# Kernel tuning notes

Measured on AMD Instinct MI355X. Metric: run time of the kernel, lower is better.

Reference implementation:

```python
import jax, jax.numpy as jnp
from jax import lax
import numpy as np

ANCHOR_SCALES = [8, 16, 32]
ANCHOR_RATIOS = [0.5, 1.0, 2.0]
NUM_ANCHOR = len(ANCHOR_SCALES) * len(ANCHOR_RATIOS)
NMS_THRESH = 0.5


def _base_anchors(base_size=16):
    # generate_anchor_in_cell (called with defaults in the torch code)
    a = []
    for s in ANCHOR_SCALES:
        for r in ANCHOR_RATIOS:
            w = base_size * s * np.sqrt(r)
            h = w / r
            xmin = base_size / 2 - w / 2
            ymin = base_size / 2 - h / 2
            a.append([xmin, ymin, xmin + w, ymin + h])
    return np.array(a, dtype=np.float32)  # (A,4)


def _anchors_in_image(H, W, feature_stride):
    base = _base_anchors(16)  # torch code uses default stride for the base cell
    gx = np.arange(0, feature_stride * W, feature_stride)
    gy = np.arange(0, feature_stride * H, feature_stride)
    gx, gy = np.meshgrid(gx, gy)
    grid = np.stack([gx.ravel(), gy.ravel(), gx.ravel(), gy.ravel()], axis=1)  # (K,4)
    anc = (grid[:, None, :] + base[None, :, :]).reshape(-1, 4)  # (K*A,4)
    return jnp.asarray(anc, dtype=jnp.float32)


def _loc2bbox(anchors, loc):
    # anchors: (N,4) xyxy; loc: (B,N,4) (dx,dy,dw,dh)
    w = anchors[:, 2] - anchors[:, 0]
    h = anchors[:, 3] - anchors[:, 1]
    cx = anchors[:, 0] + 0.5 * w
    cy = anchors[:, 1] + 0.5 * h
    dx, dy, dw, dh = loc[..., 0], loc[..., 1], loc[..., 2], loc[..., 3]
    ncx = dx * w + cx
    ncy = dy * h + cy
    nw = jnp.exp(dw) * w
    nh = jnp.exp(dh) * h
    return jnp.stack([ncx - 0.5 * nw, ncy - 0.5 * nh,
                      ncx + 0.5 * nw, ncy + 0.5 * nh], axis=-1)


def _clip_bbox(rois, img_h, img_w):
    x = jnp.clip(rois[..., 0::2], 0.0, img_w)
    y = jnp.clip(rois[..., 1::2], 0.0, img_h)
    out = jnp.stack([x[..., 0], y[..., 0], x[..., 1], y[..., 1]], axis=-1)
    return out


def _nms(boxes, scores, thresh):
    # Greedy NMS. Returns (boxes_sorted_by_score, keep_mask) of fixed shape.
    N = boxes.shape[0]
    order = jnp.argsort(-scores)
    b = boxes[order]
    x1, y1, x2, y2 = b[:, 0], b[:, 1], b[:, 2], b[:, 3]
    areas = (x2 - x1) * (y2 - y1)
    idx = jnp.arange(N)

    def body(i, state):
        suppressed, keep = state
        cur = jnp.logical_not(suppressed[i])
        keep = keep.at[i].set(cur)
        bi = b[i]
        xx1 = jnp.maximum(bi[0], x1)
        yy1 = jnp.maximum(bi[1], y1)
        xx2 = jnp.minimum(bi[2], x2)
        yy2 = jnp.minimum(bi[3], y2)
        inter = jnp.maximum(xx2 - xx1, 0.0) * jnp.maximum(yy2 - yy1, 0.0)
        iou = inter / (areas[i] + areas - inter)
        sup = (iou > thresh) & cur & (idx > i)
        return (suppressed | sup, keep)

    suppressed0 = jnp.zeros((N,), dtype=bool)
    keep0 = jnp.zeros((N,), dtype=bool)
    _, keep = lax.fori_loop(0, N, body, (suppressed0, keep0))
    return b, keep, order


def reference(feature_map, feature_stride, conv_w, conv_b, score_w, score_b, loc_w, loc_b):
    B, C, H, W = feature_map.shape
    anchors = _anchors_in_image(H, W, feature_stride)  # (H*W*A, 4)

    dn = ('NCHW', 'OIHW', 'NCHW')
    mid = jax.nn.relu(lax.conv_general_dilated(
        feature_map, conv_w, (1, 1), ((1, 1), (1, 1)), dimension_numbers=dn)
        + conv_b[None, :, None, None])
    rpn_score = lax.conv_general_dilated(mid, score_w, (1, 1), ((0, 0), (0, 0)),
                                         dimension_numbers=dn) + score_b[None, :, None, None]
    rpn_loc = lax.conv_general_dilated(mid, loc_w, (1, 1), ((0, 0), (0, 0)),
                                       dimension_numbers=dn) + loc_b[None, :, None, None]

    # NCHW -> NHWC -> (B,H,W,A,2), softmax over the 2 classes
    rpn_score = jnp.transpose(rpn_score, (0, 2, 3, 1)).reshape(B, H, W, NUM_ANCHOR, 2)
    rpn_score = jax.nn.softmax(rpn_score, axis=4)
    rpn_loc = jnp.transpose(rpn_loc, (0, 2, 3, 1)).reshape(B, -1, 4)
    rpn_fg_score = rpn_score[..., 1].reshape(B, -1)
    rpn_score = rpn_score.reshape(B, -1, 2)

    rois = _loc2bbox(anchors, rpn_loc)                      # (B,N,4)
    rois = _clip_bbox(rois, H * feature_stride, W * feature_stride)

    # torch code flattens scores across batch -> effectively B == 1
    flat_rois = rois.reshape(-1, 4)
    flat_scores = rpn_fg_score.reshape(-1)
    b_sorted, keep, _ = _nms(lax.stop_gradient(flat_rois),
                             lax.stop_gradient(flat_scores), NMS_THRESH)
    # compacted kept rois (kept first, zero padding) at fixed shape
    order = jnp.argsort(-flat_scores)
    comp = jnp.argsort(~keep)  # stable: kept positions first
    rois_out = (flat_rois[order][comp] * keep[comp][:, None].astype(flat_rois.dtype))

    return rois_out, keep[comp], anchors, rpn_loc, rpn_score


def setup_inputs() -> dict:
    key = jax.random.key(0)
    k1, k2, k3, k4 = jax.random.split(key, 4)
    C_in, C_mid, A = 2048, 256, NUM_ANCHOR
    H, W = 38, 50
    feature_map = jax.random.normal(k1, (1, C_in, H, W), dtype=jnp.float32)
    conv_w = jax.random.normal(k2, (C_mid, C_in, 3, 3), dtype=jnp.float32) * 0.01
    conv_b = jnp.zeros((C_mid,), dtype=jnp.float32)
    score_w = jax.random.normal(k3, (A * 2, C_mid, 1, 1), dtype=jnp.float32) * 0.01
    score_b = jnp.zeros((A * 2,), dtype=jnp.float32)
    loc_w = jax.random.normal(k4, (A * 4, C_mid, 1, 1), dtype=jnp.float32) * 0.01
    loc_b = jnp.zeros((A * 4,), dtype=jnp.float32)
    return {"feature_map": feature_map, "feature_stride": 16,
            "conv_w": conv_w, "conv_b": conv_b,
            "score_w": score_w, "score_b": score_b,
            "loc_w": loc_w, "loc_b": loc_b}
```

## Files before the change

kernel.cpp:

```cpp
#include <hip/hip_runtime.h>
#include <cstdint>

#define U64 unsigned long long

static constexpr int H = 38, W = 50, P = 1900;
static constexpr int CIN = 2048, CMID = 256;
static constexpr int NA = 9, NBOX = 17100;
static constexpr int HP = 40, WP = 52, QP = HP * WP;
static constexpr int TPITCH = 2084;
static constexpr int KS = 7;
static constexpr int NW = 268;
static constexpr int PITCH = 17152;
static constexpr float NMS_T = 0.5f;
static constexpr int QTILE = 256;

static constexpr size_t SZ_INT  = (size_t)CIN * TPITCH * 4;
static constexpr size_t SZ_WT   = (size_t)9 * CIN * CMID * 4;
static constexpr size_t SZ_PART = (size_t)KS * P * CMID * 4;
static constexpr size_t OFF_INT  = 0;
static constexpr size_t OFF_WT   = OFF_INT + SZ_INT;
static constexpr size_t OFF_PART = OFF_WT + SZ_WT;
static constexpr size_t REGA     = OFF_PART + SZ_PART;
static constexpr size_t OFF_MASK = 0;
static constexpr size_t OFF_MID  = REGA;
static constexpr size_t OFF_FG   = OFF_MID + 1945600;
static constexpr size_t OFF_BOX  = OFF_FG + 68608;
static constexpr size_t OFF_SBOX = OFF_BOX + 273664;
static constexpr size_t OFF_SAREA= OFF_SBOX + 273664;
static constexpr size_t OFF_CNT  = OFF_SAREA + 68608;
static constexpr size_t WS_NEED  = OFF_CNT + 68608;

__device__ __forceinline__ U64 rdlane64(U64 v, int l) {
    unsigned lo = (unsigned)__builtin_amdgcn_readlane((int)(unsigned)(v & 0xffffffffull), l);
    unsigned hi = (unsigned)__builtin_amdgcn_readlane((int)(unsigned)(v >> 32), l);
    return ((U64)hi << 32) | (U64)lo;
}


__global__ __launch_bounds__(256) void k_sentinel(float* out, int n) {
    int i = blockIdx.x * 256 + threadIdx.x;
    if (i < n) out[i] = 1.2345678e8f;
}

__global__ __launch_bounds__(256) void k_in_t(const float* __restrict__ fm, float* __restrict__ in_tT) {
    int idx = blockIdx.x * 256 + threadIdx.x;
    if (idx >= CIN * (H * W)) return;
    int ci = idx / (H * W), hw = idx - ci * (H * W);
    int h = hw / W, w = hw - h * W;
    in_tT[(size_t)ci * TPITCH + (h + 1) * WP + 1 + w] = fm[idx];
}

__global__ __launch_bounds__(256) void k_w_t(const float* __restrict__ cw, float* __restrict__ w2) {
    int idx = blockIdx.x * 256 + threadIdx.x;
    if (idx >= CMID * CIN * 9) return;
    int co = idx / (CIN * 9);
    int rem = idx - co * (CIN * 9);
    int ci = rem / 9, k = rem - ci * 9;
    w2[((size_t)(co >> 3) * CIN + ci) * 72 + k * 8 + (co & 7)] = cw[idx];
}

__global__ __launch_bounds__(256, 2) void k_conv(const float* __restrict__ in_tT,
                                                 const float* __restrict__ w2,
                                                 float* __restrict__ partial) {
    __shared__ float4 s_in4[16 * 104];
    int t = threadIdx.x;
    int lane = t & 63;
    int sub = __builtin_amdgcn_readfirstlane(t >> 6);

    int raw = blockIdx.x;
    int xcd = raw & 7, i0 = raw >> 3;
    int L = xcd * 63 + i0;
    int z = L / 72;
    int r0 = L - z * 72;
    int bx = r0 % 9, by = r0 / 9;
    int q0 = bx * QTILE;
    int cout0 = by * 32;
    int cin0 = (z <= 1) ? 304 * z : 608 + 288 * (z - 2);
    int cin1 = cin0 + ((z <= 1) ? 304 : 288);

    float acc[4][8];
#pragma unroll
    for (int j = 0; j < 4; ++j)
#pragma unroll
        for (int c = 0; c < 8; ++c) acc[j][c] = 0.f;

    const float* wbase = w2 + (size_t)(by * 4 + sub) * CIN * 72;

    for (int c0 = cin0; c0 < cin1; c0 += 16) {
        for (int idx = t; idx < 16 * 92; idx += 256) {
            int r = idx / 92, j = idx - r * 92;
            int qf = q0 - 56 + 4 * j;
            float4 v = make_float4(0.f, 0.f, 0.f, 0.f);
            if (qf >= 0 && qf <= 2080)
                v = *reinterpret_cast<const float4*>(in_tT + (size_t)(c0 + r) * TPITCH + qf);
            s_in4[r * 104 + j + (j >> 3)] = v;
        }
        __syncthreads();
#pragma unroll 1
        for (int r = 0; r < 16; ++r) {
            const float4* row4 = s_in4 + r * 104;
            const float4* w4 = reinterpret_cast<const float4*>(wbase + (size_t)(c0 + r) * 72);
#pragma unroll
            for (int dy = 0; dy < 3; ++dy) {
                int v0 = lane + 13 * dy;
                int v1 = v0 + 1, v2 = v0 + 2;
                float4 F0 = row4[v0 + (v0 >> 3)];
                float4 F1 = row4[v1 + (v1 >> 3)];
                float4 F2 = row4[v2 + (v2 >> 3)];
                float F[12] = {F0.x, F0.y, F0.z, F0.w, F1.x, F1.y, F1.z, F1.w,
                               F2.x, F2.y, F2.z, F2.w};
#pragma unroll
                for (int dxi = 0; dxi < 3; ++dxi) {
                    int k = dy * 3 + dxi;
                    float4 wa = w4[k * 2], wb = w4[k * 2 + 1];
                    float wv[8] = {wa.x, wa.y, wa.z, wa.w, wb.x, wb.y, wb.z, wb.w};
#pragma unroll
                    for (int jj = 0; jj < 4; ++jj) {
                        float iv = F[jj + dxi + 3];
#pragma unroll
                        for (int c = 0; c < 8; ++c) acc[jj][c] += iv * wv[c];
                    }
                }
            }
        }
        __syncthreads();
    }
    float* part = partial + (size_t)z * P * CMID;
#pragma unroll
    for (int jj = 0; jj < 4; ++jj) {
        int q = q0 + 4 * lane + jj;
        if (q < QP) {
            int hp = q / WP, wp_ = q - hp * WP;
            if (hp >= 1 && hp <= H && wp_ >= 1 && wp_ <= W) {
                int p = (hp - 1) * W + (wp_ - 1);
                float* dst = part + (size_t)p * CMID + cout0 + sub * 8;
                float4* d4 = reinterpret_cast<float4*>(dst);
                d4[0] = make_float4(acc[jj][0], acc[jj][1], acc[jj][2], acc[jj][3]);
                d4[1] = make_float4(acc[jj][4], acc[jj][5], acc[jj][6], acc[jj][7]);
            }
        }
    }
}

__global__ __launch_bounds__(256) void k_reduce(const float* __restrict__ partial,
                                                const float* __restrict__ bias,
                                                float* __restrict__ mid) {
    int p = blockIdx.x, c = threadIdx.x;
    float s = bias[c];
    for (int ks = 0; ks < KS; ++ks) s += partial[(size_t)ks * P * CMID + (size_t)p * CMID + c];
    mid[(size_t)p * CMID + c] = fmaxf(s, 0.f);
}

__global__ __launch_bounds__(256) void k_heads(const float* __restrict__ mid,
                                               const float* __restrict__ score_w,
                                               const float* __restrict__ score_b,
                                               const float* __restrict__ loc_w,
                                               const float* __restrict__ loc_b,
                                               float* __restrict__ score_out,
                                               float* __restrict__ loc_out,
                                               float* __restrict__ anch_out,
                                               float* __restrict__ fg,
                                               float* __restrict__ boxes) {
    __shared__ float wl[256][56];
    __shared__ float bias[56];
    __shared__ float dots[4][64];
    int t = threadIdx.x;
    for (int idx = t; idx < 18 * 256; idx += 256) {
        int c = idx >> 8, i = idx & 255;
        wl[i][c] = score_w[idx];
    }
    for (int idx = t; idx < 36 * 256; idx += 256) {
        int c = idx >> 8, i = idx & 255;
        wl[i][18 + c] = loc_w[idx];
    }
    if (t < 18) bias[t] = score_b[t];
    else if (t < 54) bias[t] = loc_b[t - 18];
    __syncthreads();

    int pl = t >> 6, c = t & 63;
    for (int rep = 0; rep < 4; ++rep) {
        int p = blockIdx.x * 16 + rep * 4 + pl;
        if (c < 54 && p < P) {
            float d = bias[c];
            const float4* mp = reinterpret_cast<const float4*>(mid + (size_t)p * CMID);
            for (int i4 = 0; i4 < 64; ++i4) {
                float4 m4 = mp[i4];
                int i = i4 * 4;
                d += m4.x * wl[i][c] + m4.y * wl[i + 1][c] + m4.z * wl[i + 2][c] + m4.w * wl[i + 3][c];
            }
            dots[pl][c] = d;
        }
        __syncthreads();
        if (c < NA && p < P) {
            int a = c;
            int idx = p * NA + a;
            float l0 = dots[pl][2 * a], l1 = dots[pl][2 * a + 1];
            float mx = fmaxf(l0, l1);
            float e0 = expf(l0 - mx), e1 = expf(l1 - mx);
            float den = e0 + e1;
            float s0 = e0 / den, s1 = e1 / den;
            score_out[(size_t)idx * 2 + 0] = s0;
            score_out[(size_t)idx * 2 + 1] = s1;
            fg[idx] = s1;
            float dx = dots[pl][18 + 4 * a + 0];
            float dy = dots[pl][18 + 4 * a + 1];
            float dw = dots[pl][18 + 4 * a + 2];
            float dh = dots[pl][18 + 4 * a + 3];
            loc_out[(size_t)idx * 4 + 0] = dx;
            loc_out[(size_t)idx * 4 + 1] = dy;
            loc_out[(size_t)idx * 4 + 2] = dw;
            loc_out[(size_t)idx * 4 + 3] = dh;
            int hh = p / W, ww = p % W;
            const double scales[3] = {8.0, 16.0, 32.0};
            const double ratios[3] = {0.5, 1.0, 2.0};
            double s = scales[a / 3], r = ratios[a % 3];
            double wb2 = 16.0 * s * sqrt(r);
            double hb = wb2 / r;
            double xmin = 8.0 - wb2 / 2.0, ymin = 8.0 - hb / 2.0;
            float b0 = (float)xmin, b1 = (float)ymin;
            float b2 = (float)(xmin + wb2), b3 = (float)(ymin + hb);
            float gx = (float)(ww * 16), gy = (float)(hh * 16);
            float a0 = gx + b0, a1 = gy + b1, a2 = gx + b2, a3 = gy + b3;
            anch_out[(size_t)idx * 4 + 0] = a0;
            anch_out[(size_t)idx * 4 + 1] = a1;
            anch_out[(size_t)idx * 4 + 2] = a2;
            anch_out[(size_t)idx * 4 + 3] = a3;
            float aw = a2 - a0, ah = a3 - a1;
            float cx = a0 + 0.5f * aw, cy = a1 + 0.5f * ah;
            float ncx = dx * aw + cx, ncy = dy * ah + cy;
            float nw = expf(dw) * aw, nh = expf(dh) * ah;
            float x1 = ncx - 0.5f * nw, y1 = ncy - 0.5f * nh;
            float x2 = ncx + 0.5f * nw, y2 = ncy + 0.5f * nh;
            x1 = fminf(fmaxf(x1, 0.f), (float)(W * 16));
            x2 = fminf(fmaxf(x2, 0.f), (float)(W * 16));
            y1 = fminf(fmaxf(y1, 0.f), (float)(H * 16));
            y2 = fminf(fmaxf(y2, 0.f), (float)(H * 16));
            float4* bp = reinterpret_cast<float4*>(boxes);
            bp[idx] = make_float4(x1, y1, x2, y2);
        }
        __syncthreads();
    }
}

static constexpr int JSL = 2144;
__global__ __launch_bounds__(256) void k_rank_part(const float* __restrict__ fg,
                                                   int* __restrict__ cntb) {
    __shared__ float4 tile[256];
    int t = threadIdx.x;
    int i = blockIdx.x * 256 + t;
    int j0 = blockIdx.y * JSL;
    int j1 = min(NBOX, j0 + JSL);
    float my = (i < NBOX) ? fg[i] : 0.f;
    int cnt = 0;
    for (int base = j0; base < j1; base += 1024) {
        int j = base + t * 4;
        float4 v = make_float4(-3.4e38f, -3.4e38f, -3.4e38f, -3.4e38f);
        if (j + 3 < j1) {
            v = *reinterpret_cast<const float4*>(fg + j);
        } else {
            if (j < j1) v.x = fg[j];
            if (j + 1 < j1) v.y = fg[j + 1];
            if (j + 2 < j1) v.z = fg[j + 2];
            if (j + 3 < j1) v.w = fg[j + 3];
        }
        __syncthreads();
        tile[t] = v;
        __syncthreads();
        if (i < NBOX) {
            for (int u = 0; u < 256; ++u) {
                float4 s = tile[u];
                int jb = base + u * 4;
                cnt += (s.x > my) || (s.x == my && jb < i);
                cnt += (s.y > my) || (s.y == my && jb + 1 < i);
                cnt += (s.z > my) || (s.z == my && jb + 2 < i);
                cnt += (s.w > my) || (s.w == my && jb + 3 < i);
            }
        }
    }
    if (i < NBOX && cnt) atomicAdd(&cntb[i], cnt);
}

__global__ __launch_bounds__(256) void k_scatter(const int* __restrict__ cntb,
                                                 const float* __restrict__ boxes,
                                                 float* __restrict__ sboxes,
                                                 float* __restrict__ sarea) {
    int i = blockIdx.x * 256 + threadIdx.x;
    if (i >= NBOX) return;
    int c = cntb[i];
    float4 b = reinterpret_cast<const float4*>(boxes)[i];
    reinterpret_cast<float4*>(sboxes)[c] = b;
    sarea[c] = (b.z - b.x) * (b.w - b.y);
}

__global__ __launch_bounds__(256) void k_maskfill(const float* __restrict__ sboxes,
                                                  const float* __restrict__ sarea,
                                                  U64* __restrict__ maskT) {
    int w = blockIdx.y;
    int i0 = blockIdx.x * 256;
    if (w < (i0 >> 6)) return;
    __shared__ float4 sb[64];
    __shared__ float sa[64];
    int t = threadIdx.x;
    if (t < 64) {
        int j = w * 64 + t;
        if (j < NBOX) {
            sb[t] = reinterpret_cast<const float4*>(sboxes)[j];
            sa[t] = sarea[j];
        } else {
            sb[t] = make_float4(0.f, 0.f, 0.f, 0.f);
            sa[t] = 0.f;
        }
    }
    __syncthreads();
    int i = i0 + t;
    if (i >= NBOX || w < (i >> 6)) return;
    float4 bi = reinterpret_cast<const float4*>(sboxes)[i];
    float ai = sarea[i];
    U64 word = 0;
#pragma unroll 4
    for (int jb = 0; jb < 64; ++jb) {
        int j = w * 64 + jb;
        float4 bj = sb[jb];
        float xx1 = fmaxf(bi.x, bj.x), yy1 = fmaxf(bi.y, bj.y);
        float xx2 = fminf(bi.z, bj.z), yy2 = fminf(bi.w, bj.w);
        float inter = fmaxf(xx2 - xx1, 0.f) * fmaxf(yy2 - yy1, 0.f);
        float iou = inter / (ai + sa[jb] - inter);
        word |= ((U64)((iou > NMS_T) && (j > i))) << jb;
    }
    maskT[(size_t)w * PITCH + i] = word;
}

__global__ __launch_bounds__(256) void k_sweep(const U64* __restrict__ maskT,
                                               const float* __restrict__ sboxes,
                                               float* __restrict__ rois_out,
                                               float* __restrict__ keep_out) {
    __shared__ U64 rem[NW];
    __shared__ int klbuf[2][64];
    __shared__ int kn[2];
    __shared__ unsigned base_s;
    int t = threadIdx.x;
    for (int u = t; u < NW; u += 256) rem[u] = 0;
    if (t == 0) { base_s = 0; kn[0] = 0; kn[1] = 0; }

    U64 dA = 0, nA = 0, dB = 0, nB = 0;
    if (t < 64) {
        int r0 = t;
        dA = maskT[(size_t)0 * PITCH + r0];
        nA = maskT[(size_t)1 * PITCH + r0];
        int r1 = 64 + t;
        dB = maskT[(size_t)1 * PITCH + r1];
        nB = maskT[(size_t)2 * PITCH + r1];
    }
    __syncthreads();

    auto body = [&](int g, U64& dR, U64& nR) {
        if (t < 64) {
            int nv = min(64, NBOX - g * 64);
            U64 vmask = (nv == 64) ? ~0ull : ((1ull << nv) - 1);
            U64 m = rem[g];
            U64 notsup = ~m & vmask;
            U64 kept = 0;
            while (notsup) {
                int i = (int)__builtin_ctzll(notsup);
                kept |= (1ull << i);
                U64 wi = rdlane64(dR, i);
                notsup &= ~(wi | (1ull << i));
            }
            int nk = __popcll(kept);
            bool mine = (kept >> t) & 1ull;

            U64 val = mine ? nR : 0;
#pragma unroll
            for (int s = 1; s < 64; s <<= 1) val |= (U64)__shfl_xor((unsigned long long)val, s, 64);
            if (t == 0 && g + 1 < NW && val) atomicOr(&rem[g + 1], val);

            if (g + 2 < NW) {
                int row = (g + 2) * 64 + t;
                dR = (row < NBOX) ? maskT[(size_t)(g + 2) * PITCH + row] : 0;
                nR = (row < NBOX && g + 3 < NW) ? maskT[(size_t)(g + 3) * PITCH + row] : 0;
            }

            unsigned base = base_s;
            if (mine) {
                unsigned pre = (unsigned)__popcll(kept & ((1ull << t) - 1));
                unsigned dst = base + pre;
                float4 bb = reinterpret_cast<const float4*>(sboxes)[g * 64 + t];
                reinterpret_cast<float4*>(rois_out)[dst] = bb;
                keep_out[dst] = 1.0f;
                klbuf[g & 1][pre] = t;
            }
            if (t == 0) {
                kn[g & 1] = nk;
                base_s = base + (unsigned)nk;
            }
        } else if (g >= 1) {
            int pb = (g - 1) & 1;
            int nkp = kn[pb];
            if (nkp) {
                const size_t colbase = (size_t)(g - 1) * 64;
                for (int w = g + 1 + (t - 64); w < NW; w += 192) {
                    const U64* col = maskT + (size_t)w * PITCH + colbase;
                    U64 acc = 0;
                    int b = 0;
                    for (; b + 3 < nkp; b += 4) {
                        U64 v0 = col[klbuf[pb][b]];
                        U64 v1 = col[klbuf[pb][b + 1]];
                        U64 v2 = col[klbuf[pb][b + 2]];
                        U64 v3 = col[klbuf[pb][b + 3]];
                        acc |= v0 | v1 | v2 | v3;
                    }
                    for (; b < nkp; ++b) acc |= col[klbuf[pb][b]];
                    if (acc) atomicOr(&rem[w], acc);
                }
            }
        }
        __syncthreads();
    };

    for (int gg = 0; gg < NW; gg += 2) {
        body(gg, dA, nA);
        body(gg + 1, dB, nB);
    }
}

extern "C" void kernel_launch(void* const* d_in, const int* in_sizes, int n_in,
                              void* d_out, int out_size, void* d_ws, size_t ws_size,
                              hipStream_t stream) {
    const float* fm      = (const float*)d_in[0];
    const float* conv_w  = (const float*)d_in[2];
    const float* conv_b  = (const float*)d_in[3];
    const float* score_w = (const float*)d_in[4];
    const float* score_b = (const float*)d_in[5];
    const float* loc_w   = (const float*)d_in[6];
    const float* loc_b   = (const float*)d_in[7];

    float* out = (float*)d_out;
    float* rois_out  = out;
    float* keep_out  = out + NBOX * 4;
    float* anch_out  = out + NBOX * 5;
    float* loc_out   = out + NBOX * 9;
    float* score_out = out + NBOX * 13;

    if (ws_size < WS_NEED) {
        k_sentinel<<<(out_size + 255) / 256, 256, 0, stream>>>(out, out_size);
        return;
    }

    char* ws = (char*)d_ws;
    float* in_tT   = (float*)(ws + OFF_INT);
    float* w2      = (float*)(ws + OFF_WT);
    float* partial = (float*)(ws + OFF_PART);
    U64*   maskT   = (U64*)(ws + OFF_MASK);
    float* mid     = (float*)(ws + OFF_MID);
    float* fg      = (float*)(ws + OFF_FG);
    float* boxes   = (float*)(ws + OFF_BOX);
    float* sboxes  = (float*)(ws + OFF_SBOX);
    float* sarea   = (float*)(ws + OFF_SAREA);
    int*   cntb    = (int*)(ws + OFF_CNT);

    hipMemsetAsync(in_tT, 0, SZ_INT, stream);
    k_in_t<<<(CIN * H * W + 255) / 256, 256, 0, stream>>>(fm, in_tT);
    k_w_t<<<(CMID * CIN * 9 + 255) / 256, 256, 0, stream>>>(conv_w, w2);
    k_conv<<<504, 256, 0, stream>>>(in_tT, w2, partial);
    k_reduce<<<P, 256, 0, stream>>>(partial, conv_b, mid);
    k_heads<<<(P + 15) / 16, 256, 0, stream>>>(mid, score_w, score_b, loc_w, loc_b,
                                               score_out, loc_out, anch_out, fg, boxes);
    hipMemsetAsync(cntb, 0, NBOX * 4, stream);
    k_rank_part<<<dim3((NBOX + 255) / 256, 8), 256, 0, stream>>>(fg, cntb);
    k_scatter<<<(NBOX + 255) / 256, 256, 0, stream>>>(cntb, boxes, sboxes, sarea);
    hipMemsetAsync(rois_out, 0, (size_t)NBOX * 5 * 4, stream);
    k_maskfill<<<dim3((NBOX + 255) / 256, NW), 256, 0, stream>>>(sboxes, sarea, maskT);
    k_sweep<<<1, 256, 0, stream>>>(maskT, sboxes, rois_out, keep_out);
}
```

Before: 852.5 us.

## Store NMS mask row-major and sweep kept rows with coalesced lane-parallel reads

Changes the IoU suppression mask from a column-major (word-major) layout to a row-major layout with a stride of 272 words per box. The single-block sweep now assigns each kept box of the previous group to a wavefront, whose lanes read consecutive words of that box's row and OR them into the shared remove mask. The old version did gathered strided column reads per word. This aims to make the serial sweep's global reads contiguous. In exchange, maskfill writes become strided by 272 words per thread, and there are many more shared-memory atomics, one per nonzero word.

```diff
diff --git a/kernel.cpp b/kernel.cpp
--- a/kernel.cpp
+++ b/kernel.cpp
@@ -10,7 +10,7 @@
 static constexpr int TPITCH = 2084;
 static constexpr int KS = 7;
 static constexpr int NW = 268;
-static constexpr int PITCH = 17152;
+static constexpr int MSTRIDE = 272;
 static constexpr float NMS_T = 0.5f;
 static constexpr int QTILE = 256;
 
@@ -294,7 +294,7 @@
 
 __global__ __launch_bounds__(256) void k_maskfill(const float* __restrict__ sboxes,
                                                   const float* __restrict__ sarea,
-                                                  U64* __restrict__ maskT) {
+                                                  U64* __restrict__ mask) {
     int w = blockIdx.y;
     int i0 = blockIdx.x * 256;
     if (w < (i0 >> 6)) return;
@@ -327,10 +327,10 @@
         float iou = inter / (ai + sa[jb] - inter);
         word |= ((U64)((iou > NMS_T) && (j > i))) << jb;
     }
-    maskT[(size_t)w * PITCH + i] = word;
-}
-
-__global__ __launch_bounds__(256) void k_sweep(const U64* __restrict__ maskT,
+    mask[(size_t)i * MSTRIDE + w] = word;
+}
+
+__global__ __launch_bounds__(256) void k_sweep(const U64* __restrict__ mask,
                                                const float* __restrict__ sboxes,
                                                float* __restrict__ rois_out,
                                                float* __restrict__ keep_out) {
@@ -344,12 +344,11 @@
 
     U64 dA = 0, nA = 0, dB = 0, nB = 0;
     if (t < 64) {
-        int r0 = t;
-        dA = maskT[(size_t)0 * PITCH + r0];
-        nA = maskT[(size_t)1 * PITCH + r0];
+        dA = mask[(size_t)t * MSTRIDE + 0];
+        nA = mask[(size_t)t * MSTRIDE + 1];
         int r1 = 64 + t;
-        dB = maskT[(size_t)1 * PITCH + r1];
-        nB = maskT[(size_t)2 * PITCH + r1];
+        dB = mask[(size_t)r1 * MSTRIDE + 1];
+        nB = mask[(size_t)r1 * MSTRIDE + 2];
     }
     __syncthreads();
 
@@ -357,8 +356,7 @@
         if (t < 64) {
             int nv = min(64, NBOX - g * 64);
             U64 vmask = (nv == 64) ? ~0ull : ((1ull << nv) - 1);
-            U64 m = rem[g];
-            U64 notsup = ~m & vmask;
+            U64 notsup = ~rem[g] & vmask;
             U64 kept = 0;
             while (notsup) {
                 int i = (int)__builtin_ctzll(notsup);
@@ -376,8 +374,8 @@
 
             if (g + 2 < NW) {
                 int row = (g + 2) * 64 + t;
-                dR = (row < NBOX) ? maskT[(size_t)(g + 2) * PITCH + row] : 0;
-                nR = (row < NBOX && g + 3 < NW) ? maskT[(size_t)(g + 3) * PITCH + row] : 0;
+                dR = (row < NBOX) ? mask[(size_t)row * MSTRIDE + (g + 2)] : 0;
+                nR = (row < NBOX && g + 3 < NW) ? mask[(size_t)row * MSTRIDE + (g + 3)] : 0;
             }
 
             unsigned base = base_s;
@@ -396,21 +394,14 @@
         } else if (g >= 1) {
             int pb = (g - 1) & 1;
             int nkp = kn[pb];
-            if (nkp) {
-                const size_t colbase = (size_t)(g - 1) * 64;
-                for (int w = g + 1 + (t - 64); w < NW; w += 192) {
-                    const U64* col = maskT + (size_t)w * PITCH + colbase;
-                    U64 acc = 0;
-                    int b = 0;
-                    for (; b + 3 < nkp; b += 4) {
-                        U64 v0 = col[klbuf[pb][b]];
-                        U64 v1 = col[klbuf[pb][b + 1]];
-                        U64 v2 = col[klbuf[pb][b + 2]];
-                        U64 v3 = col[klbuf[pb][b + 3]];
-                        acc |= v0 | v1 | v2 | v3;
-                    }
-                    for (; b < nkp; ++b) acc |= col[klbuf[pb][b]];
-                    if (acc) atomicOr(&rem[w], acc);
+            int wv = (t >> 6) - 1;
+            int lane = t & 63;
+            for (int j = wv; j < nkp; j += 3) {
+                int row = (g - 1) * 64 + klbuf[pb][j];
+                const U64* rp = mask + (size_t)row * MSTRIDE;
+                for (int w = g + 1 + lane; w < NW; w += 64) {
+                    U64 v = rp[w];
+                    if (v) atomicOr(&rem[w], v);
                 }
             }
         }
@@ -450,7 +441,7 @@
     float* in_tT   = (float*)(ws + OFF_INT);
     float* w2      = (float*)(ws + OFF_WT);
     float* partial = (float*)(ws + OFF_PART);
-    U64*   maskT   = (U64*)(ws + OFF_MASK);
+    U64*   mask    = (U64*)(ws + OFF_MASK);
     float* mid     = (float*)(ws + OFF_MID);
     float* fg      = (float*)(ws + OFF_FG);
     float* boxes   = (float*)(ws + OFF_BOX);
@@ -469,6 +460,6 @@
     k_rank_part<<<dim3((NBOX + 255) / 256, 8), 256, 0, stream>>>(fg, cntb);
     k_scatter<<<(NBOX + 255) / 256, 256, 0, stream>>>(cntb, boxes, sboxes, sarea);
     hipMemsetAsync(rois_out, 0, (size_t)NBOX * 5 * 4, stream);
-    k_maskfill<<<dim3((NBOX + 255) / 256, NW), 256, 0, stream>>>(sboxes, sarea, maskT);
-    k_sweep<<<1, 256, 0, stream>>>(maskT, sboxes, rois_out, keep_out);
-}
+    k_maskfill<<<dim3((NBOX + 255) / 256, NW), 256, 0, stream>>>(sboxes, sarea, mask);
+    k_sweep<<<1, 256, 0, stream>>>(mask, sboxes, rois_out, keep_out);
+}
```

Measured after the change: 940.4 us. 1.1x slower.
